# Kernel optimization log

Hardware: AMD Instinct MI355X
Metric: run time of the kernel (lower is better)

## Reference

```python
import jax, jax.numpy as jnp
import numpy as np

BATCH, CHANNELS, WINDOW, N_PATCHES = 16, 64, 200, 30
D_MODEL = 256
HIDDEN = D_MODEL // 2  # 128


def setup_inputs() -> dict:
    key = jax.random.key(0)
    ks = jax.random.split(key, 7)
    s = 1.0 / np.sqrt(HIDDEN)
    return {
        "x": jax.random.normal(ks[0], (BATCH, CHANNELS, WINDOW, N_PATCHES), dtype=jnp.float32),
        "W_ih": jax.random.normal(ks[1], (4 * HIDDEN, CHANNELS), dtype=jnp.float32) * s,
        "W_hh": jax.random.normal(ks[2], (4 * HIDDEN, HIDDEN), dtype=jnp.float32) * s,
        "b_ih": jax.random.normal(ks[3], (4 * HIDDEN,), dtype=jnp.float32) * s,
        "b_hh": jax.random.normal(ks[4], (4 * HIDDEN,), dtype=jnp.float32) * s,
        "W_fc": jax.random.normal(ks[5], (CHANNELS, HIDDEN), dtype=jnp.float32) * s,
        "b_fc": jax.random.normal(ks[6], (CHANNELS,), dtype=jnp.float32) * s,
    }


def _lstm_last_h(x_seq, W_ih, W_hh, b_ih, b_hh):
    # x_seq: (N, T, C) -> final hidden state (N, H). PyTorch gate order: i, f, g, o.
    N = x_seq.shape[0]
    H = W_hh.shape[1]
    # Precompute input contribution for all timesteps: (N, T, 4H)
    xg = jnp.einsum('ntc,gc->ntg', x_seq, W_ih) + b_ih + b_hh
    xg_t = jnp.swapaxes(xg, 0, 1)  # (T, N, 4H)

    def step(carry, xt):
        h, c = carry
        gates = xt + h @ W_hh.T  # (N, 4H)
        i, f, g, o = jnp.split(gates, 4, axis=-1)
        i = jax.nn.sigmoid(i)
        f = jax.nn.sigmoid(f)
        g = jnp.tanh(g)
        o = jax.nn.sigmoid(o)
        c = f * c + i * g
        h = o * jnp.tanh(c)
        return (h, c), None

    h0 = jnp.zeros((N, H), dtype=x_seq.dtype)
    c0 = jnp.zeros((N, H), dtype=x_seq.dtype)
    (h_T, _), _ = jax.lax.scan(step, (h0, c0), xg_t)
    return h_T


def reference(x, W_ih, W_hh, b_ih, b_hh, W_fc, b_fc):
    batch, channels, window, n_patches = x.shape
    # (B, C, T, P) -> (B, P, T, C) -> (B*P, T, C): each patch is an LSTM sequence
    x_flat = jnp.transpose(x, (0, 3, 2, 1)).reshape(batch * n_patches, window, channels)
    h_last = _lstm_last_h(x_flat, W_ih, W_hh, b_ih, b_hh)  # (B*P, H)
    out = h_last @ W_fc.T + b_fc  # (B*P, C)
    return out.reshape(batch, n_patches, channels)
```

## Files before the change

kernel.cpp:

```cpp
#include <hip/hip_runtime.h>

#define BATCH 16
#define CH    64
#define TLEN  200
#define NP    30
#define HID   128
#define NSEQ  (BATCH * NP)
#define HP    144
#define H8P   160
#define XP    72
#define XGW   520

typedef _Float16 half8 __attribute__((ext_vector_type(8)));
typedef float    f32x4 __attribute__((ext_vector_type(4)));
typedef int      i32x8 __attribute__((ext_vector_type(8)));
typedef unsigned char u8;

__device__ __forceinline__ float sigm_fast(float x) {
    return __builtin_amdgcn_rcpf(1.0f + __expf(-x));
}
__device__ __forceinline__ float tanh_fast(float x) {
    return 1.0f - 2.0f * __builtin_amdgcn_rcpf(__expf(2.0f * x) + 1.0f);
}
__device__ __forceinline__ half8 cvt8(float4 a, float4 b) {
    return (half8){(_Float16)a.x,(_Float16)a.y,(_Float16)a.z,(_Float16)a.w,
                   (_Float16)b.x,(_Float16)b.y,(_Float16)b.z,(_Float16)b.w};
}

#define MFMA16(A,B,C) __builtin_amdgcn_mfma_f32_16x16x32_f16((A),(B),(C),0,0,0)
#define MFMA8(A,B,C) __builtin_amdgcn_mfma_scale_f32_16x16x128_f8f6f4((A),(B),(C),0,0,0,127,0,127)

__global__ __launch_bounds__(512, 2) void fused_lstm(
    const float* __restrict__ x, const float* __restrict__ W_ih,
    const float* __restrict__ W_hh, const float* __restrict__ b_ih,
    const float* __restrict__ b_hh, const float* __restrict__ W_fc,
    const float* __restrict__ b_fc, float* __restrict__ out)
{
    const int tid = threadIdx.x;
    const int w  = tid >> 6;
    const int l  = tid & 63;
    const int lr = l & 15;
    const int lq = l >> 4;

    const int blk  = blockIdx.x;
    const int pair = (blk & 7) * 30 + (blk >> 3);
    const int n0 = pair * 2;
    const int b0 = n0 / NP;
    const int p0 = n0 % NP;

    __shared__ __align__(16) _Float16 hz[5][HP];
    __shared__ __align__(16) u8       hz8[5][H8P];
    __shared__ __align__(16) _Float16 xlds[TLEN][2][XP];
    __shared__ __align__(16) float    xgb[2][16 * XGW];

    i32x8 b8i, b8f, b8o;
    {
        const int Ts[3] = {0, 1, 3};
        i32x8* dst[3] = {&b8i, &b8f, &b8o};
#pragma unroll
        for (int q = 0; q < 3; ++q) {
            const float* rw = W_hh + (size_t)(128*Ts[q] + 16*w + lr) * HID + 32*lq;
            i32x8 pk;
#pragma unroll
            for (int r = 0; r < 8; ++r) {
                int v = __builtin_amdgcn_cvt_pk_fp8_f32(rw[4*r],     rw[4*r + 1], 0, false);
                v     = __builtin_amdgcn_cvt_pk_fp8_f32(rw[4*r + 2], rw[4*r + 3], v, true);
                pk[r] = v;
            }
            *dst[q] = pk;
        }
    }
    half8 bg16[4];
    {
        const float* rh = W_hh + (size_t)(128*2 + 16*w + lr) * HID;
#pragma unroll
        for (int kt = 0; kt < 4; ++kt) {
            const int k0 = 32*kt + 8*lq;
            bg16[kt] = cvt8(*(const float4*)(rh + k0), *(const float4*)(rh + k0 + 4));
        }
    }
    half8 bih[4][2];
    float biasx[4];
#pragma unroll
    for (int T = 0; T < 4; ++T) {
        const int g = 128*T + 16*w + lr;
        const float* ri = W_ih + (size_t)g * CH;
#pragma unroll
        for (int j = 0; j < 2; ++j) {
            const int k0 = 32*j + 8*lq;
            bih[T][j] = cvt8(*(const float4*)(ri + k0), *(const float4*)(ri + k0 + 4));
        }
        biasx[T] = b_ih[g] + b_hh[g];
    }

    if (tid < (5 * HP) / 2) ((unsigned*)hz)[tid] = 0u;
    if (tid < (5 * H8P) / 4) ((unsigned*)hz8)[tid] = 0u;

    for (int e = tid; e < CH * TLEN; e += 512) {
        const int t = e % TLEN, c = e / TLEN;
        const float* src = x + ((size_t)(b0 * CH + c) * TLEN + t) * NP + p0;
        float2 v = *(const float2*)src;
        xlds[t][0][c] = (_Float16)v.x;
        xlds[t][1][c] = (_Float16)v.y;
    }
    float cst = 0.f;
    const int hcol = 16*w + lr;
    const int r0 = (lr == 0) ? 0 : (lr == 4) ? 1 : 4;
    const int r1 = (lr == 0) ? 2 : (lr == 4) ? 3 : 4;
    const _Float16* hpA  = &hz[r0][8 * lq];
    const _Float16* hpB  = &hz[r1][8 * lq];
    const u8*       hp8A = &hz8[r0][32 * lq];
    const u8*       hp8B = &hz8[r1][32 * lq];
    __syncthreads();

#define XG_BURST(P, TB) {                                                         \
        const _Float16* xr_ = &xlds[8*(P) + (lr >> 1)][lr & 1][8*lq];             \
        half8 xf0_ = *(const half8*)xr_;                                          \
        half8 xf1_ = *(const half8*)(xr_ + 32);                                   \
        f32x4 g0_ = {biasx[0], biasx[0], biasx[0], biasx[0]};                     \
        f32x4 g1_ = {biasx[1], biasx[1], biasx[1], biasx[1]};                     \
        f32x4 g2_ = {biasx[2], biasx[2], biasx[2], biasx[2]};                     \
        f32x4 g3_ = {biasx[3], biasx[3], biasx[3], biasx[3]};                     \
        g0_ = MFMA16(xf0_, bih[0][0], g0_); g0_ = MFMA16(xf1_, bih[0][1], g0_);   \
        g1_ = MFMA16(xf0_, bih[1][0], g1_); g1_ = MFMA16(xf1_, bih[1][1], g1_);   \
        g2_ = MFMA16(xf0_, bih[2][0], g2_); g2_ = MFMA16(xf1_, bih[2][1], g2_);   \
        g3_ = MFMA16(xf0_, bih[3][0], g3_); g3_ = MFMA16(xf1_, bih[3][1], g3_);   \
        _Pragma("unroll") for (int r_ = 0; r_ < 4; ++r_) {                        \
            float* dst_ = &xgb[TB][(4*lq + r_) * XGW + hcol * 4];                 \
            *(f32x4*)dst_ = (f32x4){g0_[r_], g1_[r_], g2_[r_], g3_[r_]};          \
        } }

    XG_BURST(0, 0)
    __syncthreads();

#pragma unroll 1
    for (int p = 0; p < 25; ++p) {
        const int pe = p & 1;
#pragma unroll
        for (int k = 0; k < 8; ++k) {
            const int cur = k & 1;
            const int nxt = cur ^ 1;
            f32x4 xg4 = *(const f32x4*)&xgb[pe][(2*k + (lq & 1)) * XGW + hcol * 4];
            i32x8 a8 = *(const i32x8*)(cur ? hp8B : hp8A);
            const _Float16* hr = cur ? hpB : hpA;
            half8 a0 = *(const half8*)(hr);
            half8 a1 = *(const half8*)(hr + 32);
            half8 a2 = *(const half8*)(hr + 64);
            half8 a3 = *(const half8*)(hr + 96);
            f32x4 zz = {0.f, 0.f, 0.f, 0.f};
            __builtin_amdgcn_s_setprio(1);
            f32x4 ci = MFMA8(a8, b8i, zz);
            f32x4 cf = MFMA8(a8, b8f, zz);
            f32x4 cg = MFMA16(a0, bg16[0], zz);
            cg = MFMA16(a1, bg16[1], cg);
            cg = MFMA16(a2, bg16[2], cg);
            cg = MFMA16(a3, bg16[3], cg);
            float si = sigm_fast(ci[0] + xg4[0]);
            float sf = sigm_fast(cf[0] + xg4[1]);
            float tg = tanh_fast(cg[0] + xg4[2]);
            float cnew = sf * cst + si * tg;
            f32x4 co = MFMA8(a8, b8o, zz);
            __builtin_amdgcn_s_setprio(0);
            if (k == 0 && p < 24) XG_BURST(p + 1, pe ^ 1)
            float hv = sigm_fast(co[0] + xg4[3]) * tanh_fast(cnew);
            cst = cnew;
            if (l < 32) {
                hz[2*nxt + lq][hcol] = (_Float16)hv;
                int hb = __builtin_amdgcn_cvt_pk_fp8_f32(hv, hv, 0, false);
                hz8[2*nxt + lq][hcol] = (u8)hb;
            }
            __syncthreads();
        }
    }

    if (tid < 2 * CH) {
        const int s = tid >> 6, ch = tid & 63;
        const float* wf = W_fc + (size_t)ch * HID;
        float acc = b_fc[ch];
#pragma unroll
        for (int j8 = 0; j8 < 16; ++j8) {
            half8 hv = *(const half8*)&hz[s][8 * j8];
            float4 w0 = *(const float4*)(wf + 8 * j8);
            float4 w1 = *(const float4*)(wf + 8 * j8 + 4);
            acc += w0.x * (float)hv[0] + w0.y * (float)hv[1]
                 + w0.z * (float)hv[2] + w0.w * (float)hv[3]
                 + w1.x * (float)hv[4] + w1.y * (float)hv[5]
                 + w1.z * (float)hv[6] + w1.w * (float)hv[7];
        }
        out[(size_t)(n0 + s) * CH + ch] = acc;
    }
}

extern "C" void kernel_launch(void* const* d_in, const int* in_sizes, int n_in,
                              void* d_out, int out_size, void* d_ws, size_t ws_size,
                              hipStream_t stream) {
    (void)in_sizes; (void)n_in; (void)out_size; (void)d_ws; (void)ws_size;
    fused_lstm<<<NSEQ / 2, 512, 0, stream>>>(
        (const float*)d_in[0], (const float*)d_in[1], (const float*)d_in[2],
        (const float*)d_in[3], (const float*)d_in[4], (const float*)d_in[5],
        (const float*)d_in[6], (float*)d_out);
}
```

Baseline: 189.1 us.

## Process one sequence per block with 4 waves each covering 32 hidden units

```diff
diff --git a/kernel.cpp b/kernel.cpp
--- a/kernel.cpp
+++ b/kernel.cpp
@@ -30,7 +30,7 @@
 #define MFMA16(A,B,C) __builtin_amdgcn_mfma_f32_16x16x32_f16((A),(B),(C),0,0,0)
 #define MFMA8(A,B,C) __builtin_amdgcn_mfma_scale_f32_16x16x128_f8f6f4((A),(B),(C),0,0,0,127,0,127)
 
-__global__ __launch_bounds__(512, 2) void fused_lstm(
+__global__ __launch_bounds__(256, 2) void fused_lstm(
     const float* __restrict__ x, const float* __restrict__ W_ih,
     const float* __restrict__ W_hh, const float* __restrict__ b_ih,
     const float* __restrict__ b_hh, const float* __restrict__ W_fc,
@@ -42,24 +42,24 @@
     const int lr = l & 15;
     const int lq = l >> 4;
 
-    const int blk  = blockIdx.x;
-    const int pair = (blk & 7) * 30 + (blk >> 3);
-    const int n0 = pair * 2;
-    const int b0 = n0 / NP;
-    const int p0 = n0 % NP;
+    const int blk = blockIdx.x;
+    const int n   = (blk & 7) * 60 + (blk >> 3);
+    const int b0  = n / NP;
+    const int p0  = n % NP;
 
     __shared__ __align__(16) _Float16 hz[5][HP];
     __shared__ __align__(16) u8       hz8[5][H8P];
-    __shared__ __align__(16) _Float16 xlds[TLEN][2][XP];
-    __shared__ __align__(16) float    xgb[2][16 * XGW];
-
-    i32x8 b8i, b8f, b8o;
+    __shared__ __align__(16) _Float16 xlds[TLEN][XP];
+    __shared__ __align__(16) float    xgb[2][8][XGW];
+
+    i32x8 b8[3][2];
     {
         const int Ts[3] = {0, 1, 3};
-        i32x8* dst[3] = {&b8i, &b8f, &b8o};
-#pragma unroll
-        for (int q = 0; q < 3; ++q) {
-            const float* rw = W_hh + (size_t)(128*Ts[q] + 16*w + lr) * HID + 32*lq;
+#pragma unroll
+        for (int q = 0; q < 3; ++q)
+#pragma unroll
+          for (int ct = 0; ct < 2; ++ct) {
+            const float* rw = W_hh + (size_t)(128*Ts[q] + 32*w + 16*ct + lr) * HID + 32*lq;
             i32x8 pk;
 #pragma unroll
             for (int r = 0; r < 8; ++r) {
@@ -67,44 +67,45 @@
                 v     = __builtin_amdgcn_cvt_pk_fp8_f32(rw[4*r + 2], rw[4*r + 3], v, true);
                 pk[r] = v;
             }
-            *dst[q] = pk;
-        }
-    }
-    half8 bg16[4];
-    {
-        const float* rh = W_hh + (size_t)(128*2 + 16*w + lr) * HID;
+            b8[q][ct] = pk;
+          }
+    }
+    half8 bg16[2][4];
+#pragma unroll
+    for (int ct = 0; ct < 2; ++ct) {
+        const float* rh = W_hh + (size_t)(256 + 32*w + 16*ct + lr) * HID;
 #pragma unroll
         for (int kt = 0; kt < 4; ++kt) {
             const int k0 = 32*kt + 8*lq;
-            bg16[kt] = cvt8(*(const float4*)(rh + k0), *(const float4*)(rh + k0 + 4));
-        }
-    }
-    half8 bih[4][2];
-    float biasx[4];
-#pragma unroll
-    for (int T = 0; T < 4; ++T) {
-        const int g = 128*T + 16*w + lr;
+            bg16[ct][kt] = cvt8(*(const float4*)(rh + k0), *(const float4*)(rh + k0 + 4));
+        }
+    }
+    half8 bih[4][2][2];
+    float biasx[4][2];
+#pragma unroll
+    for (int T = 0; T < 4; ++T)
+#pragma unroll
+      for (int ct = 0; ct < 2; ++ct) {
+        const int g = 128*T + 32*w + 16*ct + lr;
         const float* ri = W_ih + (size_t)g * CH;
 #pragma unroll
         for (int j = 0; j < 2; ++j) {
             const int k0 = 32*j + 8*lq;
-            bih[T][j] = cvt8(*(const float4*)(ri + k0), *(const float4*)(ri + k0 + 4));
-        }
-        biasx[T] = b_ih[g] + b_hh[g];
-    }
+            bih[T][ct][j] = cvt8(*(const float4*)(ri + k0), *(const float4*)(ri + k0 + 4));
+        }
+        biasx[T][ct] = b_ih[g] + b_hh[g];
+      }
 
     if (tid < (5 * HP) / 2) ((unsigned*)hz)[tid] = 0u;
     if (tid < (5 * H8P) / 4) ((unsigned*)hz8)[tid] = 0u;
 
-    for (int e = tid; e < CH * TLEN; e += 512) {
+    for (int e = tid; e < CH * TLEN; e += 256) {
         const int t = e % TLEN, c = e / TLEN;
-        const float* src = x + ((size_t)(b0 * CH + c) * TLEN + t) * NP + p0;
-        float2 v = *(const float2*)src;
-        xlds[t][0][c] = (_Float16)v.x;
-        xlds[t][1][c] = (_Float16)v.y;
+        xlds[t][c] = (_Float16)x[((size_t)(b0 * CH + c) * TLEN + t) * NP + p0];
     }
     float cst = 0.f;
-    const int hcol = 16*w + lr;
+    const int ct1 = lq & 1;
+    const int hid = 32*w + 16*ct1 + lr;
     const int r0 = (lr == 0) ? 0 : (lr == 4) ? 1 : 4;
     const int r1 = (lr == 0) ? 2 : (lr == 4) ? 3 : 4;
     const _Float16* hpA  = &hz[r0][8 * lq];
@@ -114,20 +115,24 @@
     __syncthreads();
 
 #define XG_BURST(P, TB) {                                                         \
-        const _Float16* xr_ = &xlds[8*(P) + (lr >> 1)][lr & 1][8*lq];             \
+        const _Float16* xr_ = &xlds[8*(P) + (lr & 7)][8*lq];                      \
         half8 xf0_ = *(const half8*)xr_;                                          \
         half8 xf1_ = *(const half8*)(xr_ + 32);                                   \
-        f32x4 g0_ = {biasx[0], biasx[0], biasx[0], biasx[0]};                     \
-        f32x4 g1_ = {biasx[1], biasx[1], biasx[1], biasx[1]};                     \
-        f32x4 g2_ = {biasx[2], biasx[2], biasx[2], biasx[2]};                     \
-        f32x4 g3_ = {biasx[3], biasx[3], biasx[3], biasx[3]};                     \
-        g0_ = MFMA16(xf0_, bih[0][0], g0_); g0_ = MFMA16(xf1_, bih[0][1], g0_);   \
-        g1_ = MFMA16(xf0_, bih[1][0], g1_); g1_ = MFMA16(xf1_, bih[1][1], g1_);   \
-        g2_ = MFMA16(xf0_, bih[2][0], g2_); g2_ = MFMA16(xf1_, bih[2][1], g2_);   \
-        g3_ = MFMA16(xf0_, bih[3][0], g3_); g3_ = MFMA16(xf1_, bih[3][1], g3_);   \
-        _Pragma("unroll") for (int r_ = 0; r_ < 4; ++r_) {                        \
-            float* dst_ = &xgb[TB][(4*lq + r_) * XGW + hcol * 4];                 \
-            *(f32x4*)dst_ = (f32x4){g0_[r_], g1_[r_], g2_[r_], g3_[r_]};          \
+        f32x4 ac_[4][2];                                                          \
+        _Pragma("unroll") for (int T_ = 0; T_ < 4; ++T_)                          \
+        { _Pragma("unroll") for (int c_ = 0; c_ < 2; ++c_) {                      \
+            f32x4 a_ = {biasx[T_][c_], biasx[T_][c_], biasx[T_][c_], biasx[T_][c_]}; \
+            a_ = MFMA16(xf0_, bih[T_][c_][0], a_);                                \
+            a_ = MFMA16(xf1_, bih[T_][c_][1], a_);                                \
+            ac_[T_][c_] = a_;                                                     \
+        } }                                                                       \
+        if (lq < 2) {                                                             \
+            _Pragma("unroll") for (int c_ = 0; c_ < 2; ++c_)                      \
+            { _Pragma("unroll") for (int r_ = 0; r_ < 4; ++r_) {                  \
+                float* dst_ = &xgb[TB][4*lq + r_][(32*w + 16*c_ + lr) * 4];       \
+                *(f32x4*)dst_ = (f32x4){ac_[0][c_][r_], ac_[1][c_][r_],           \
+                                        ac_[2][c_][r_], ac_[3][c_][r_]};          \
+            } }                                                                   \
         } }
 
     XG_BURST(0, 0)
@@ -140,7 +145,7 @@
         for (int k = 0; k < 8; ++k) {
             const int cur = k & 1;
             const int nxt = cur ^ 1;
-            f32x4 xg4 = *(const f32x4*)&xgb[pe][(2*k + (lq & 1)) * XGW + hcol * 4];
+            f32x4 xg4 = *(const f32x4*)&xgb[pe][k][hid * 4];
             i32x8 a8 = *(const i32x8*)(cur ? hp8B : hp8A);
             const _Float16* hr = cur ? hpB : hpA;
             half8 a0 = *(const half8*)(hr);
@@ -149,37 +154,50 @@
             half8 a3 = *(const half8*)(hr + 96);
             f32x4 zz = {0.f, 0.f, 0.f, 0.f};
             __builtin_amdgcn_s_setprio(1);
-            f32x4 ci = MFMA8(a8, b8i, zz);
-            f32x4 cf = MFMA8(a8, b8f, zz);
-            f32x4 cg = MFMA16(a0, bg16[0], zz);
-            cg = MFMA16(a1, bg16[1], cg);
-            cg = MFMA16(a2, bg16[2], cg);
-            cg = MFMA16(a3, bg16[3], cg);
-            float si = sigm_fast(ci[0] + xg4[0]);
-            float sf = sigm_fast(cf[0] + xg4[1]);
-            float tg = tanh_fast(cg[0] + xg4[2]);
+            f32x4 ci0 = MFMA8(a8, b8[0][0], zz);
+            f32x4 ci1 = MFMA8(a8, b8[0][1], zz);
+            f32x4 cf0 = MFMA8(a8, b8[1][0], zz);
+            f32x4 cf1 = MFMA8(a8, b8[1][1], zz);
+            f32x4 cg0 = MFMA16(a0, bg16[0][0], zz);
+            cg0 = MFMA16(a1, bg16[0][1], cg0);
+            cg0 = MFMA16(a2, bg16[0][2], cg0);
+            cg0 = MFMA16(a3, bg16[0][3], cg0);
+            f32x4 cg1 = MFMA16(a0, bg16[1][0], zz);
+            cg1 = MFMA16(a1, bg16[1][1], cg1);
+            cg1 = MFMA16(a2, bg16[1][2], cg1);
+            cg1 = MFMA16(a3, bg16[1][3], cg1);
+            float gi = (ct1 ? ci1[0] : ci0[0]) + xg4[0];
+            float gf = (ct1 ? cf1[0] : cf0[0]) + xg4[1];
+            float gg = (ct1 ? cg1[0] : cg0[0]) + xg4[2];
+            float si = sigm_fast(gi);
+            float sf = sigm_fast(gf);
+            float tg = tanh_fast(gg);
             float cnew = sf * cst + si * tg;
-            f32x4 co = MFMA8(a8, b8o, zz);
+            f32x4 co0 = MFMA8(a8, b8[2][0], zz);
+            f32x4 co1 = MFMA8(a8, b8[2][1], zz);
             __builtin_amdgcn_s_setprio(0);
             if (k == 0 && p < 24) XG_BURST(p + 1, pe ^ 1)
-            float hv = sigm_fast(co[0] + xg4[3]) * tanh_fast(cnew);
+            float hv = sigm_fast((ct1 ? co1[0] : co0[0]) + xg4[3]) * tanh_fast(cnew);
             cst = cnew;
             if (l < 32) {
-                hz[2*nxt + lq][hcol] = (_Float16)hv;
-                int hb = __builtin_amdgcn_cvt_pk_fp8_f32(hv, hv, 0, false);
-                hz8[2*nxt + lq][hcol] = (u8)hb;
+                _Float16 hh = (_Float16)hv;
+                hz[2*nxt][hid]     = hh;
+                hz[2*nxt + 1][hid] = hh;
+                u8 hb = (u8)__builtin_amdgcn_cvt_pk_fp8_f32(hv, hv, 0, false);
+                hz8[2*nxt][hid]     = hb;
+                hz8[2*nxt + 1][hid] = hb;
             }
             __syncthreads();
         }
     }
 
-    if (tid < 2 * CH) {
-        const int s = tid >> 6, ch = tid & 63;
+    if (tid < CH) {
+        const int ch = tid;
         const float* wf = W_fc + (size_t)ch * HID;
         float acc = b_fc[ch];
 #pragma unroll
         for (int j8 = 0; j8 < 16; ++j8) {
-            half8 hv = *(const half8*)&hz[s][8 * j8];
+            half8 hv = *(const half8*)&hz[0][8 * j8];
             float4 w0 = *(const float4*)(wf + 8 * j8);
             float4 w1 = *(const float4*)(wf + 8 * j8 + 4);
             acc += w0.x * (float)hv[0] + w0.y * (float)hv[1]
@@ -187,7 +205,7 @@
                  + w1.x * (float)hv[4] + w1.y * (float)hv[5]
                  + w1.z * (float)hv[6] + w1.w * (float)hv[7];
         }
-        out[(size_t)(n0 + s) * CH + ch] = acc;
+        out[(size_t)n * CH + ch] = acc;
     }
 }
 
@@ -195,7 +213,7 @@
                               void* d_out, int out_size, void* d_ws, size_t ws_size,
                               hipStream_t stream) {
     (void)in_sizes; (void)n_in; (void)out_size; (void)d_ws; (void)ws_size;
-    fused_lstm<<<NSEQ / 2, 512, 0, stream>>>(
+    fused_lstm<<<NSEQ, 256, 0, stream>>>(
         (const float*)d_in[0], (const float*)d_in[1], (const float*)d_in[2],
         (const float*)d_in[3], (const float*)d_in[4], (const float*)d_in[5],
         (const float*)d_in[6], (float*)d_out);
```

New measurement: 241.6 us. 1.28x slower.

## Assign one LSTM sequence per block instead of two

Applied to the files above, without the earlier changes.

```diff
diff --git a/kernel.cpp b/kernel.cpp
--- a/kernel.cpp
+++ b/kernel.cpp
@@ -30,7 +30,7 @@
 #define MFMA16(A,B,C) __builtin_amdgcn_mfma_f32_16x16x32_f16((A),(B),(C),0,0,0)
 #define MFMA8(A,B,C) __builtin_amdgcn_mfma_scale_f32_16x16x128_f8f6f4((A),(B),(C),0,0,0,127,0,127)
 
-__global__ __launch_bounds__(512, 2) void fused_lstm(
+__global__ __launch_bounds__(512, 4) void fused_lstm(
     const float* __restrict__ x, const float* __restrict__ W_ih,
     const float* __restrict__ W_hh, const float* __restrict__ b_ih,
     const float* __restrict__ b_hh, const float* __restrict__ W_fc,
@@ -42,16 +42,15 @@
     const int lr = l & 15;
     const int lq = l >> 4;
 
-    const int blk  = blockIdx.x;
-    const int pair = (blk & 7) * 30 + (blk >> 3);
-    const int n0 = pair * 2;
-    const int b0 = n0 / NP;
-    const int p0 = n0 % NP;
+    const int blk = blockIdx.x;
+    const int n   = (blk & 7) * 60 + (blk >> 3);
+    const int b0  = n / NP;
+    const int p0  = n % NP;
 
-    __shared__ __align__(16) _Float16 hz[5][HP];
-    __shared__ __align__(16) u8       hz8[5][H8P];
-    __shared__ __align__(16) _Float16 xlds[TLEN][2][XP];
-    __shared__ __align__(16) float    xgb[2][16 * XGW];
+    __shared__ __align__(16) _Float16 hz[3][HP];
+    __shared__ __align__(16) u8       hz8[3][H8P];
+    __shared__ __align__(16) _Float16 xlds[TLEN][XP];
+    __shared__ __align__(16) float    xgb[2][8][XGW];
 
     i32x8 b8i, b8f, b8o;
     {
@@ -72,7 +71,7 @@
     }
     half8 bg16[4];
     {
-        const float* rh = W_hh + (size_t)(128*2 + 16*w + lr) * HID;
+        const float* rh = W_hh + (size_t)(256 + 16*w + lr) * HID;
 #pragma unroll
         for (int kt = 0; kt < 4; ++kt) {
             const int k0 = 32*kt + 8*lq;
@@ -93,41 +92,38 @@
         biasx[T] = b_ih[g] + b_hh[g];
     }
 
-    if (tid < (5 * HP) / 2) ((unsigned*)hz)[tid] = 0u;
-    if (tid < (5 * H8P) / 4) ((unsigned*)hz8)[tid] = 0u;
+    if (tid < (3 * HP) / 2) ((unsigned*)hz)[tid] = 0u;
+    if (tid < (3 * H8P) / 4) ((unsigned*)hz8)[tid] = 0u;
 
     for (int e = tid; e < CH * TLEN; e += 512) {
         const int t = e % TLEN, c = e / TLEN;
-        const float* src = x + ((size_t)(b0 * CH + c) * TLEN + t) * NP + p0;
-        float2 v = *(const float2*)src;
-        xlds[t][0][c] = (_Float16)v.x;
-        xlds[t][1][c] = (_Float16)v.y;
+        xlds[t][c] = (_Float16)x[((size_t)(b0 * CH + c) * TLEN + t) * NP + p0];
     }
     float cst = 0.f;
     const int hcol = 16*w + lr;
-    const int r0 = (lr == 0) ? 0 : (lr == 4) ? 1 : 4;
-    const int r1 = (lr == 0) ? 2 : (lr == 4) ? 3 : 4;
-    const _Float16* hpA  = &hz[r0][8 * lq];
-    const _Float16* hpB  = &hz[r1][8 * lq];
-    const u8*       hp8A = &hz8[r0][32 * lq];
-    const u8*       hp8B = &hz8[r1][32 * lq];
+    const _Float16* hpA  = &hz[(lr == 0) ? 0 : 2][8 * lq];
+    const _Float16* hpB  = &hz[(lr == 0) ? 1 : 2][8 * lq];
+    const u8*       hp8A = &hz8[(lr == 0) ? 0 : 2][32 * lq];
+    const u8*       hp8B = &hz8[(lr == 0) ? 1 : 2][32 * lq];
     __syncthreads();
 
 #define XG_BURST(P, TB) {                                                         \
-        const _Float16* xr_ = &xlds[8*(P) + (lr >> 1)][lr & 1][8*lq];             \
+        const _Float16* xr_ = &xlds[8*(P) + (lr & 7)][8*lq];                      \
         half8 xf0_ = *(const half8*)xr_;                                          \
         half8 xf1_ = *(const half8*)(xr_ + 32);                                   \
-        f32x4 g0_ = {biasx[0], biasx[0], biasx[0], biasx[0]};                     \
-        f32x4 g1_ = {biasx[1], biasx[1], biasx[1], biasx[1]};                     \
-        f32x4 g2_ = {biasx[2], biasx[2], biasx[2], biasx[2]};                     \
-        f32x4 g3_ = {biasx[3], biasx[3], biasx[3], biasx[3]};                     \
-        g0_ = MFMA16(xf0_, bih[0][0], g0_); g0_ = MFMA16(xf1_, bih[0][1], g0_);   \
-        g1_ = MFMA16(xf0_, bih[1][0], g1_); g1_ = MFMA16(xf1_, bih[1][1], g1_);   \
-        g2_ = MFMA16(xf0_, bih[2][0], g2_); g2_ = MFMA16(xf1_, bih[2][1], g2_);   \
-        g3_ = MFMA16(xf0_, bih[3][0], g3_); g3_ = MFMA16(xf1_, bih[3][1], g3_);   \
-        _Pragma("unroll") for (int r_ = 0; r_ < 4; ++r_) {                        \
-            float* dst_ = &xgb[TB][(4*lq + r_) * XGW + hcol * 4];                 \
-            *(f32x4*)dst_ = (f32x4){g0_[r_], g1_[r_], g2_[r_], g3_[r_]};          \
+        f32x4 ac_[4];                                                             \
+        _Pragma("unroll") for (int T_ = 0; T_ < 4; ++T_) {                        \
+            f32x4 a_ = {biasx[T_], biasx[T_], biasx[T_], biasx[T_]};              \
+            a_ = MFMA16(xf0_, bih[T_][0], a_);                                    \
+            a_ = MFMA16(xf1_, bih[T_][1], a_);                                    \
+            ac_[T_] = a_;                                                         \
+        }                                                                         \
+        if (lq < 2) {                                                             \
+            _Pragma("unroll") for (int r_ = 0; r_ < 4; ++r_) {                    \
+                float* dst_ = &xgb[TB][4*lq + r_][hcol * 4];                      \
+                *(f32x4*)dst_ = (f32x4){ac_[0][r_], ac_[1][r_],                   \
+                                        ac_[2][r_], ac_[3][r_]};                  \
+            }                                                                     \
         } }
 
     XG_BURST(0, 0)
@@ -140,7 +136,7 @@
         for (int k = 0; k < 8; ++k) {
             const int cur = k & 1;
             const int nxt = cur ^ 1;
-            f32x4 xg4 = *(const f32x4*)&xgb[pe][(2*k + (lq & 1)) * XGW + hcol * 4];
+            f32x4 xg4 = *(const f32x4*)&xgb[pe][k][hcol * 4];
             i32x8 a8 = *(const i32x8*)(cur ? hp8B : hp8A);
             const _Float16* hr = cur ? hpB : hpA;
             half8 a0 = *(const half8*)(hr);
@@ -164,22 +160,21 @@
             if (k == 0 && p < 24) XG_BURST(p + 1, pe ^ 1)
             float hv = sigm_fast(co[0] + xg4[3]) * tanh_fast(cnew);
             cst = cnew;
-            if (l < 32) {
-                hz[2*nxt + lq][hcol] = (_Float16)hv;
-                int hb = __builtin_amdgcn_cvt_pk_fp8_f32(hv, hv, 0, false);
-                hz8[2*nxt + lq][hcol] = (u8)hb;
+            if (l < 16) {
+                hz[nxt][hcol] = (_Float16)hv;
+                hz8[nxt][hcol] = (u8)__builtin_amdgcn_cvt_pk_fp8_f32(hv, hv, 0, false);
             }
             __syncthreads();
         }
     }
 
-    if (tid < 2 * CH) {
-        const int s = tid >> 6, ch = tid & 63;
+    if (tid < CH) {
+        const int ch = tid;
         const float* wf = W_fc + (size_t)ch * HID;
         float acc = b_fc[ch];
 #pragma unroll
         for (int j8 = 0; j8 < 16; ++j8) {
-            half8 hv = *(const half8*)&hz[s][8 * j8];
+            half8 hv = *(const half8*)&hz[0][8 * j8];
             float4 w0 = *(const float4*)(wf + 8 * j8);
             float4 w1 = *(const float4*)(wf + 8 * j8 + 4);
             acc += w0.x * (float)hv[0] + w0.y * (float)hv[1]
@@ -187,7 +182,7 @@
                  + w1.x * (float)hv[4] + w1.y * (float)hv[5]
                  + w1.z * (float)hv[6] + w1.w * (float)hv[7];
         }
-        out[(size_t)(n0 + s) * CH + ch] = acc;
+        out[(size_t)n * CH + ch] = acc;
     }
 }
 
@@ -195,7 +190,7 @@
                               void* d_out, int out_size, void* d_ws, size_t ws_size,
                               hipStream_t stream) {
     (void)in_sizes; (void)n_in; (void)out_size; (void)d_ws; (void)ws_size;
-    fused_lstm<<<NSEQ / 2, 512, 0, stream>>>(
+    fused_lstm<<<NSEQ, 512, 0, stream>>>(
         (const float*)d_in[0], (const float*)d_in[1], (const float*)d_in[2],
         (const float*)d_in[3], (const float*)d_in[4], (const float*)d_in[5],
         (const float*)d_in[6], (float*)d_out);
```

After: 267.4 us. +41.4%, slower.
